# Kernel optimization log

Measured on AMD Instinct MI355X. Metric: run time of the kernel, lower is better.

## Reference

```python
import jax, jax.numpy as jnp
import numpy as np

N = 50000      # nodes
E = 800000     # edges (avg degree 16)
DIN = 256      # input_dim
DH = 128       # hidden_dim
ALPHA_LOGIT = 0.6190392084062235  # logit(0.65)


def setup_inputs() -> dict:
    key = jax.random.key(0)
    ks = jax.random.split(key, 12)
    f = lambda k, s: jax.random.normal(k, s, dtype=jnp.float32)
    return {
        "x": f(ks[0], (N, DIN)),
        "edge_index": jax.random.randint(ks[1], (2, E), 0, N, dtype=jnp.int32),
        "reranker_scores": f(ks[2], (N,)),
        # input_proj
        "Wp": f(ks[3], (DIN, DH)) * 0.02, "bp": jnp.zeros((DH,), jnp.float32),
        # SAGEConv 0: lin_l (aggregated neighbors, with bias), lin_r (root, no bias)
        "Wl0": f(ks[4], (DIN, DH)) * 0.02, "bl0": jnp.zeros((DH,), jnp.float32),
        "Wr0": f(ks[5], (DIN, DH)) * 0.02,
        # SAGEConv 1
        "Wl1": f(ks[6], (DH, DH)) * 0.02, "bl1": jnp.zeros((DH,), jnp.float32),
        "Wr1": f(ks[7], (DH, DH)) * 0.02,
        # score head MLP
        "W1": f(ks[8], (DH, DH // 2)) * 0.02, "b1": jnp.zeros((DH // 2,), jnp.float32),
        "W2": f(ks[9], (DH // 2, 1)) * 0.02, "b2": jnp.zeros((1,), jnp.float32),
        "alpha_logit": jnp.float32(ALPHA_LOGIT),
    }


def _sage_conv(h, src, dst, Wl, bl, Wr):
    # PyG SAGEConv (aggr='mean', root_weight=True):
    # out = lin_l(mean_{j in N(i)} h_j) + lin_r(h_i)
    msg = h[src]                                             # [E, d] gather
    agg = jax.ops.segment_sum(msg, dst, num_segments=N)      # [N, d]
    cnt = jax.ops.segment_sum(jnp.ones((src.shape[0],), h.dtype), dst, num_segments=N)
    agg = agg / jnp.maximum(cnt, 1.0)[:, None]               # mean; isolated nodes -> 0
    return agg @ Wl + bl + h @ Wr


def reference(x, edge_index, reranker_scores, Wp, bp, Wl0, bl0, Wr0,
              Wl1, bl1, Wr1, W1, b1, W2, b2, alpha_logit):
    src, dst = edge_index[0], edge_index[1]
    # norm_type='none' -> no input normalization; eval mode -> dropout is identity
    residual = x @ Wp + bp                                   # [N, DH]
    h = jax.nn.relu(_sage_conv(x, src, dst, Wl0, bl0, Wr0)) + residual
    h = jax.nn.relu(_sage_conv(h, src, dst, Wl1, bl1, Wr1)) + h
    gnn_scores = (jax.nn.relu(h @ W1 + b1) @ W2 + b2)[:, 0]  # [N]
    alpha = jax.nn.sigmoid(alpha_logit)
    return alpha * reranker_scores + (1.0 - alpha) * gnn_scores
```

## Files before the change

kernel.cpp:

```cpp
#include <hip/hip_runtime.h>
#include <hip/hip_bf16.h>


#define DIN 256
#define DH 128
#define NPB 256
#define LOG_NPB 8
#define NBMAX 256
#define EPB 2048
#define JL (EPB/256)
#define SLOTS 8192

typedef __attribute__((ext_vector_type(8))) short short8;
typedef __attribute__((ext_vector_type(4))) float float4v;
typedef __attribute__((ext_vector_type(2))) float float2v;

__device__ inline ushort f2b(float f){
  unsigned u = __float_as_uint(f);
  u = (u + 0x7fffu + ((u >> 16) & 1u)) >> 16;
  return (ushort)u;
}
__device__ inline float blo(unsigned v){ return __uint_as_float(v << 16); }
__device__ inline float bhi(unsigned v){ return __uint_as_float(v & 0xffff0000u); }
__device__ inline short8 pack8(float4 f0, float4 f1){
  short8 v;
  v[0]=(short)f2b(f0.x); v[1]=(short)f2b(f0.y); v[2]=(short)f2b(f0.z); v[3]=(short)f2b(f0.w);
  v[4]=(short)f2b(f1.x); v[5]=(short)f2b(f1.y); v[6]=(short)f2b(f1.z); v[7]=(short)f2b(f1.w);
  return v;
}
__device__ inline void glds16(const ushort* g, ushort* l){
  __builtin_amdgcn_global_load_lds((const __attribute__((address_space(1))) void*)g,
                                   (__attribute__((address_space(3))) void*)l, 16, 0, 0);
}
__device__ inline unsigned char enc8(float v){
  return (unsigned char)(__builtin_amdgcn_cvt_pk_fp8_f32(v, v, 0, false) & 0xFF);
}
__device__ inline float2v dec8(unsigned u){
  return __builtin_amdgcn_cvt_pk_f32_fp8((int)u, false);
}

__device__ inline void gather16x2(const ushort* __restrict__ a8,
    const int* __restrict__ adj, int pA, int eA, int pB, int eB, int lane,
    float2v& aA, float2v& aB)
{
  while (pA < eA || pB < eB){
    ushort uA[16], uB[16];
    bool dA = pA < eA, dB = pB < eB;
    if (dA){
      #pragma unroll
      for (int j=0;j<16;j++){
        int ix = __builtin_amdgcn_readfirstlane(adj[pA+j]);
        uA[j] = a8[(size_t)ix*64 + lane];
      }
    }
    if (dB){
      #pragma unroll
      for (int j=0;j<16;j++){
        int ix = __builtin_amdgcn_readfirstlane(adj[pB+j]);
        uB[j] = a8[(size_t)ix*64 + lane];
      }
    }
    if (dA){
      #pragma unroll
      for (int j=0;j<16;j++) aA += dec8(uA[j]);
      pA += 16;
    }
    if (dB){
      #pragma unroll
      for (int j=0;j<16;j++) aB += dec8(uB[j]);
      pB += 16;
    }
  }
}

__global__ __launch_bounds__(256) void fused_front(
    const float* __restrict__ x, int N, ushort* __restrict__ xb, int nstripe,
    const float* __restrict__ Wp, const float* __restrict__ Wl0, const float* __restrict__ Wr0,
    const float* __restrict__ Wl1, const float* __restrict__ Wr1, const float* __restrict__ W1,
    ushort* __restrict__ Wpf, ushort* __restrict__ Wl0f, ushort* __restrict__ Wr0f,
    ushort* __restrict__ Wl1f, ushort* __restrict__ Wr1f, ushort* __restrict__ W1f,
    const int* __restrict__ src, const int* __restrict__ dst, int E, int NB,
    int* __restrict__ bucketCnt, int* __restrict__ pairS, int* __restrict__ pairD,
    int nPart, int nConv)
{
  __shared__ int hist[NBMAX], lbase[NBMAX], gbase[NBMAX], lcur[NBMAX], sc[NBMAX];
  __shared__ int ls[EPB], ld[EPB];
  int bid = blockIdx.x;
  int t = threadIdx.x;

  if (bid < nPart){
    int base = bid * EPB;
    int cntE = E - base; if (cntE > EPB) cntE = EPB;
    for (int i=t;i<NB;i+=256) hist[i]=0;
    __syncthreads();
    int myS[JL], myD[JL];
    #pragma unroll
    for (int j=0;j<JL;j++){
      int e = base + j*256 + t;
      if (e < E){ myS[j]=src[e]; myD[j]=dst[e]; atomicAdd(&hist[myD[j]>>LOG_NPB],1); }
      else myD[j] = -1;
    }
    __syncthreads();
    if (t < NBMAX) sc[t] = (t < NB)? hist[t] : 0;
    __syncthreads();
    for (int st=1; st<NBMAX; st<<=1){
      int v = 0;
      if (t < NBMAX && t >= st) v = sc[t-st];
      __syncthreads();
      if (t < NBMAX) sc[t] += v;
      __syncthreads();
    }
    if (t < NB){
      int excl = (t>0)? sc[t-1] : 0;
      lbase[t] = excl; lcur[t] = excl;
      gbase[t] = atomicAdd(&bucketCnt[t], hist[t]);
    }
    __syncthreads();
    #pragma unroll
    for (int j=0;j<JL;j++){
      if (myD[j] >= 0){
        int b = myD[j] >> LOG_NPB;
        int p = atomicAdd(&lcur[b], 1);
        ls[p] = myS[j]; ld[p] = myD[j];
      }
    }
    __syncthreads();
    for (int i=t;i<cntE;i+=256){
      int d = ld[i];
      int b = d >> LOG_NPB;
      int p = gbase[b] + (i - lbase[b]);
      if (p < SLOTS){
        pairS[(size_t)b*SLOTS + p] = ls[i];
        pairD[(size_t)b*SLOTS + p] = d;
      }
    }
  } else if (bid < nPart + nConv){
    int gi = (bid - nPart)*256 + t;
    if (gi < nstripe*512){
      int L = gi & 63, ks = (gi>>6)&7, s = gi>>9;
      int row = s*16 + (L&15);
      int k = ks*32 + (L>>4)*8;
      short8 v;
      if (row < N){
        const float* p = x + (size_t)row*DIN + k;
        v = pack8(*(const float4*)p, *(const float4*)(p+4));
      } else {
        #pragma unroll
        for (int j=0;j<8;j++) v[j]=0;
      }
      *(short8*)(xb + (size_t)gi*8) = v;
    }
  } else {
    int gi = (bid - nPart - nConv)*256 + t;
    if (gi < 17408){
      const float* sw; ushort* dw; int cols, b0;
      if      (gi <  4096){ sw=Wp;  dw=Wpf;  cols=128; b0=0; }
      else if (gi <  8192){ sw=Wl0; dw=Wl0f; cols=128; b0=4096; }
      else if (gi < 12288){ sw=Wr0; dw=Wr0f; cols=128; b0=8192; }
      else if (gi < 14336){ sw=Wl1; dw=Wl1f; cols=128; b0=12288; }
      else if (gi < 16384){ sw=Wr1; dw=Wr1f; cols=128; b0=14336; }
      else                { sw=W1;  dw=W1f;  cols=64;  b0=16384; }
      int i = gi - b0;
      int ln = i & 63, g = i >> 6;
      int ntq = cols >> 4;
      int nt = g % ntq, ks = g / ntq;
      int col = nt*16 + (ln & 15);
      int k0 = ks*32 + (ln >> 4)*8;
      short8 v;
      #pragma unroll
      for (int j=0;j<8;j++) v[j] = (short)f2b(sw[(size_t)(k0+j)*cols + col]);
      *(short8*)(dw + (size_t)i*8) = v;
    }
  }
}

__global__ __launch_bounds__(256) void gemm0_csr(
    const ushort* __restrict__ xb, int N, int nstripe, int ngemm, int nbuck,
    const ushort* __restrict__ Wpf, const ushort* __restrict__ Wl0f, const ushort* __restrict__ Wr0f,
    const float* __restrict__ bp,
    ushort* __restrict__ xp, unsigned char* __restrict__ q8, ushort* __restrict__ xr0,
    const int* __restrict__ bucketCnt, const int* __restrict__ pairS, const int* __restrict__ pairD,
    int* __restrict__ off, int* __restrict__ deg, int* __restrict__ adj)
{
  __shared__ __align__(16) ushort smem[32768];
  int bid = blockIdx.x, t = threadIdx.x;

  if (bid >= nbuck){
    int g = bid - nbuck;
    int xcd = g & 7, jj = g >> 3;
    int mat = jj % 3;
    int b = xcd + 8*(jj/3);
    int nblk = ngemm / 3;
    const ushort* Wf = (mat==0)? Wpf : (mat==1)? Wl0f : Wr0f;
    int w = t>>6, lane = t&63, lq = lane&15, quad = lane>>4;
    #pragma unroll
    for (int j=0;j<16;j++){
      int gg = w + j*4;
      glds16(Wf + (size_t)gg*512 + lane*8, smem + gg*512);
    }
    __syncthreads();
    float bias[8];
    #pragma unroll
    for (int nt=0;nt<8;nt++) bias[nt] = (mat==0)? bp[nt*16 + lq] : 0.f;
    int nchunk = (nstripe + 3) >> 2;

#define LOADAV(AV, cc) do { \
    int stripe_ = (cc)*4 + w; \
    if (stripe_ < nstripe){ \
      _Pragma("unroll") \
      for (int ks=0;ks<8;ks++) \
        AV[ks] = *(const short8*)(xb + ((size_t)stripe_*8 + ks)*512 + lane*8); \
    } \
  } while(0)

#define COMPSTORE(AV, cc) do { \
    int stripe_ = (cc)*4 + w; \
    if (stripe_ < nstripe){ \
      int row0_ = stripe_*16; \
      float4v acc_[8]; \
      _Pragma("unroll") for (int nt=0;nt<8;nt++){ \
        _Pragma("unroll") for (int r=0;r<4;r++) acc_[nt][r]=0.f; } \
      _Pragma("unroll") for (int ks=0;ks<8;ks++){ \
        _Pragma("unroll") for (int nt=0;nt<8;nt++){ \
          short8 bf_ = *(const short8*)(smem + (size_t)((ks*8+nt)*64 + lane)*8); \
          acc_[nt] = __builtin_amdgcn_mfma_f32_16x16x32_bf16(AV[ks], bf_, acc_[nt], 0,0,0); \
        } \
      } \
      if (mat == 1){ \
        _Pragma("unroll") for (int nt=0;nt<8;nt++) \
        _Pragma("unroll") for (int r=0;r<4;r++){ \
          int row_ = row0_ + quad*4 + r; \
          if (row_ < N) q8[(size_t)row_*128 + nt*16 + lq] = enc8(acc_[nt][r]); \
        } \
      } else { \
        ushort* Y_ = (mat==0)? xp : xr0; \
        _Pragma("unroll") for (int nt=0;nt<8;nt++) \
        _Pragma("unroll") for (int r=0;r<4;r++){ \
          int row_ = row0_ + quad*4 + r; \
          if (row_ < N) Y_[(size_t)row_*128 + nt*16 + lq] = f2b(acc_[nt][r] + bias[nt]); \
        } \
      } \
    } \
  } while(0)

    short8 avA[8], avB[8];
    int c = b;
    if (c < nchunk){
      LOADAV(avA, c);
      while (true){
        int cn = c + nblk;
        if (cn < nchunk) LOADAV(avB, cn);
        COMPSTORE(avA, c);
        c = cn;
        if (c >= nchunk) break;
        cn = c + nblk;
        if (cn < nchunk) LOADAV(avA, cn);
        COMPSTORE(avB, c);
        c = cn;
        if (c >= nchunk) break;
      }
    }
#undef LOADAV
#undef COMPSTORE
  } else {
    int b = bid;
    int* cnt  = (int*)smem;
    int* offl = cnt + 256;
    int* s1   = offl + 257;
    int* win  = s1 + 256;
    int node0 = b * NPB;
    int base  = b * SLOTS;
    int ce = bucketCnt[b]; if (ce > SLOTS) ce = SLOTS;
    int ce4 = ce & ~3;
    cnt[t] = 0;
    __syncthreads();
    for (int i = t*4; i < ce4; i += 1024){
      int4 dd = *(const int4*)(pairD + base + i);
      atomicAdd(&cnt[dd.x - node0], 1);
      atomicAdd(&cnt[dd.y - node0], 1);
      atomicAdd(&cnt[dd.z - node0], 1);
      atomicAdd(&cnt[dd.w - node0], 1);
    }
    for (int i = ce4 + t; i < ce; i += 256)
      atomicAdd(&cnt[pairD[(size_t)base+i] - node0], 1);
    __syncthreads();
    int a = cnt[t];
    int pa = (a + 15) & ~15;
    s1[t] = pa;
    __syncthreads();
    for (int st=1; st<256; st<<=1){
      int v = (t>=st)? s1[t-st] : 0;
      __syncthreads();
      s1[t] += v;
      __syncthreads();
    }
    int excl = (t>0)? s1[t-1] : 0;
    offl[t] = excl;
    int ptotal = s1[255]; if (ptotal > SLOTS) ptotal = SLOTS;
    int node = node0 + t;
    if (node < N){ off[node] = base + excl; deg[node] = a; }
    __syncthreads();
    for (int i=t;i<ptotal;i+=256) win[i] = N;
    __syncthreads();
    for (int i = t*4; i < ce4; i += 1024){
      int4 dd = *(const int4*)(pairD + base + i);
      int4 ss = *(const int4*)(pairS + base + i);
      int p0 = atomicAdd(&offl[dd.x - node0], 1); if (p0 < SLOTS) win[p0] = ss.x;
      int p1 = atomicAdd(&offl[dd.y - node0], 1); if (p1 < SLOTS) win[p1] = ss.y;
      int p2 = atomicAdd(&offl[dd.z - node0], 1); if (p2 < SLOTS) win[p2] = ss.z;
      int p3 = atomicAdd(&offl[dd.w - node0], 1); if (p3 < SLOTS) win[p3] = ss.w;
    }
    for (int i = ce4 + t; i < ce; i += 256){
      int dd = pairD[(size_t)base+i];
      int p = atomicAdd(&offl[dd - node0], 1);
      if (p < SLOTS) win[p] = pairS[(size_t)base+i];
    }
    __syncthreads();
    for (int i=t;i<ptotal;i+=256) adj[(size_t)base+i] = win[i];
  }
}

__global__ __launch_bounds__(256) void combine0_f8(
    const unsigned char* __restrict__ agg8, const ushort* __restrict__ rootsrc,
    const ushort* __restrict__ ressrc, const float* __restrict__ bias,
    const int* __restrict__ off, const int* __restrict__ deg,
    const int* __restrict__ adj, ushort* __restrict__ out, int n)
{
  int t = threadIdx.x;
  int d = t & 63, w = t >> 6;
  int nA = blockIdx.x*8 + w*2, nB = nA + 1;
  if (nA >= n) return;
  const ushort* a8 = (const ushort*)agg8;
  bool vB = nB < n;
  unsigned rtA = ((const unsigned*)rootsrc)[(size_t)nA*64 + d];
  unsigned rsA = ((const unsigned*)ressrc)[(size_t)nA*64 + d];
  unsigned rtB = 0, rsB = 0;
  int pA = off[nA], cA = deg[nA], eA = pA + ((cA + 15) & ~15);
  int pB = 0, cB = 0, eB = 0;
  if (vB){
    rtB = ((const unsigned*)rootsrc)[(size_t)nB*64 + d];
    rsB = ((const unsigned*)ressrc)[(size_t)nB*64 + d];
    pB = off[nB]; cB = deg[nB]; eB = pB + ((cB + 15) & ~15);
  }
  float2v aA = {0.f, 0.f}, aB = {0.f, 0.f};
  gather16x2(a8, adj, pA, eA, pB, eB, d, aA, aB);
  float b0 = bias[2*d], b1v = bias[2*d+1];
  float invA = 1.f / (float)((cA > 1)? cA : 1);
  float o0 = fmaxf(aA[0]*invA + b0  + blo(rtA), 0.f) + blo(rsA);
  float o1 = fmaxf(aA[1]*invA + b1v + bhi(rtA), 0.f) + bhi(rsA);
  ((unsigned*)out)[(size_t)nA*64 + d] = (unsigned)f2b(o0) | ((unsigned)f2b(o1) << 16);
  if (vB){
    float invB = 1.f / (float)((cB > 1)? cB : 1);
    float q0 = fmaxf(aB[0]*invB + b0  + blo(rtB), 0.f) + blo(rsB);
    float q1 = fmaxf(aB[1]*invB + b1v + bhi(rtB), 0.f) + bhi(rsB);
    ((unsigned*)out)[(size_t)nB*64 + d] = (unsigned)f2b(q0) | ((unsigned)f2b(q1) << 16);
  }
}

__global__ __launch_bounds__(256) void gemm1_wres(
    const ushort* __restrict__ h, int N,
    const ushort* __restrict__ Wl1f, const ushort* __restrict__ Wr1f,
    unsigned char* __restrict__ q8, ushort* __restrict__ hr1)
{
  __shared__ __align__(16) ushort Bs[32768];
  int t = threadIdx.x, w = t>>6, lane = t&63, lq = lane&15, quad = lane>>4;
  int tile = blockIdx.x;
  #pragma unroll
  for (int j=0;j<16;j++){
    int r = w + j*4;
    int m = r>>5, g = r&31;
    const ushort* Wm = m ? Wr1f : Wl1f;
    glds16(Wm + (size_t)g*512 + lane*8, Bs + r*512);
  }
  short8 av[2][4];
  int row0 = tile*128 + w*32;
  #pragma unroll
  for (int mt=0;mt<2;mt++){
    int row = row0 + mt*16 + lq; if (row >= N) row = N-1;
    #pragma unroll
    for (int ks=0;ks<4;ks++)
      av[mt][ks] = *(const short8*)(h + (size_t)row*128 + ks*32 + quad*8);
  }
  __syncthreads();
  #pragma unroll
  for (int m=0;m<2;m++){
    float4v acc[2][8];
    #pragma unroll
    for (int i=0;i<2;i++)
      #pragma unroll
      for (int j=0;j<8;j++)
        #pragma unroll
        for (int r=0;r<4;r++) acc[i][j][r] = 0.f;
    #pragma unroll
    for (int ks=0;ks<4;ks++){
      #pragma unroll
      for (int nt=0;nt<8;nt++){
        short8 bf = *(const short8*)(Bs + ((m*32 + ks*8 + nt)*64 + lane)*8);
        acc[0][nt] = __builtin_amdgcn_mfma_f32_16x16x32_bf16(av[0][ks], bf, acc[0][nt], 0,0,0);
        acc[1][nt] = __builtin_amdgcn_mfma_f32_16x16x32_bf16(av[1][ks], bf, acc[1][nt], 0,0,0);
      }
    }
    #pragma unroll
    for (int mt=0;mt<2;mt++){
      #pragma unroll
      for (int r=0;r<4;r++){
        int row = row0 + mt*16 + quad*4 + r;
        if (row < N){
          if (m == 0){
            #pragma unroll
            for (int nt=0;nt<8;nt++)
              q8[(size_t)row*128 + nt*16 + lq] = enc8(acc[mt][nt][r]);
          } else {
            #pragma unroll
            for (int nt=0;nt<8;nt++)
              hr1[(size_t)row*128 + nt*16 + lq] = f2b(acc[mt][nt][r]);
          }
        }
      }
    }
  }
}

__global__ __launch_bounds__(256) void combine1_head(
    const unsigned char* __restrict__ agg8, const ushort* __restrict__ hr1,
    const ushort* __restrict__ h, const float* __restrict__ bl1,
    const int* __restrict__ off, const int* __restrict__ deg, const int* __restrict__ adj,
    const ushort* __restrict__ W1f, const float* __restrict__ b1,
    const float* __restrict__ W2, const float* __restrict__ b2,
    const float* __restrict__ alogit, const float* __restrict__ rer,
    float* __restrict__ out, int n)
{
  __shared__ __align__(16) ushort W1s[8192];
  __shared__ __align__(16) ushort h2s[16*136];
  int t = threadIdx.x, w = t>>6, lane = t&63, lq = lane&15, quad = lane>>4;
  #pragma unroll
  for (int j=0;j<4;j++){
    int g = w + j*4;
    glds16(W1f + (size_t)g*512 + lane*8, W1s + g*512);
  }
  int node0 = blockIdx.x*16;
  unsigned* h2u = (unsigned*)h2s;
  const ushort* a8 = (const ushort*)agg8;
  float bb0 = bl1[2*lane], bb1 = bl1[2*lane+1];
  #pragma unroll
  for (int jp=0;jp<2;jp++){
    int nA = node0 + w*4 + jp*2, nB = nA + 1;
    bool vA = nA < n, vB = nB < n;
    unsigned rtA=0, rsA=0, rtB=0, rsB=0;
    int pA=0, eA=0, cA=0, pB=0, eB=0, cB=0;
    if (vA){
      rtA = ((const unsigned*)hr1)[(size_t)nA*64 + lane];
      rsA = ((const unsigned*)h  )[(size_t)nA*64 + lane];
      pA = off[nA]; cA = deg[nA]; eA = pA + ((cA + 15) & ~15);
    }
    if (vB){
      rtB = ((const unsigned*)hr1)[(size_t)nB*64 + lane];
      rsB = ((const unsigned*)h  )[(size_t)nB*64 + lane];
      pB = off[nB]; cB = deg[nB]; eB = pB + ((cB + 15) & ~15);
    }
    float2v aA = {0.f, 0.f}, aB = {0.f, 0.f};
    gather16x2(a8, adj, pA, eA, pB, eB, lane, aA, aB);
    float o0A=0.f, o1A=0.f, o0B=0.f, o1B=0.f;
    if (vA){
      float inv = 1.f / (float)((cA > 1)? cA : 1);
      o0A = fmaxf(aA[0]*inv + bb0 + blo(rtA), 0.f) + blo(rsA);
      o1A = fmaxf(aA[1]*inv + bb1 + bhi(rtA), 0.f) + bhi(rsA);
    }
    if (vB){
      float inv = 1.f / (float)((cB > 1)? cB : 1);
      o0B = fmaxf(aB[0]*inv + bb0 + blo(rtB), 0.f) + blo(rsB);
      o1B = fmaxf(aB[1]*inv + bb1 + bhi(rtB), 0.f) + bhi(rsB);
    }
    h2u[(w*4 + jp*2    )*68 + lane] = (unsigned)f2b(o0A) | ((unsigned)f2b(o1A) << 16);
    h2u[(w*4 + jp*2 + 1)*68 + lane] = (unsigned)f2b(o0B) | ((unsigned)f2b(o1B) << 16);
  }
  __syncthreads();

  short8 av[4];
  #pragma unroll
  for (int ks=0;ks<4;ks++)
    av[ks] = *(const short8*)(h2s + lq*136 + ks*32 + quad*8);
  float4v acc[4];
  #pragma unroll
  for (int nt=0;nt<4;nt++)
    #pragma unroll
    for (int r=0;r<4;r++) acc[nt][r] = 0.f;
  #pragma unroll
  for (int ks=0;ks<4;ks++){
    #pragma unroll
    for (int nt=0;nt<4;nt++){
      short8 bf = *(const short8*)(W1s + ((ks*4 + nt)*64 + lane)*8);
      acc[nt] = __builtin_amdgcn_mfma_f32_16x16x32_bf16(av[ks], bf, acc[nt], 0,0,0);
    }
  }
  float al = alogit[0];
  float a  = 1.f / (1.f + __expf(-al));
  float pw[4] = {0.f,0.f,0.f,0.f};
  #pragma unroll
  for (int nt=0; nt<4; nt++){
    int c = nt*16 + lq;
    float w2 = W2[c];
    float bb = b1[c];
    #pragma unroll
    for (int r=0; r<4; r++)
      pw[r] += fmaxf(acc[nt][r] + bb, 0.f) * w2;
  }
  #pragma unroll
  for (int mask=1; mask<16; mask<<=1){
    #pragma unroll
    for (int r=0; r<4; r++)
      pw[r] += __shfl_xor(pw[r], mask);
  }
  if (lq == 0){
    #pragma unroll
    for (int r=0; r<4; r++){
      int rl = quad*4 + r;
      if ((rl >> 2) == w){
        int node = node0 + rl;
        if (node < n)
          out[node] = a * rer[node] + (1.f - a) * (pw[r] + b2[0]);
      }
    }
  }
}

extern "C" void kernel_launch(void* const* d_in, const int* in_sizes, int n_in,
                              void* d_out, int out_size, void* d_ws, size_t ws_size,
                              hipStream_t stream)
{
  (void)n_in; (void)out_size; (void)ws_size;
  const float* x    = (const float*)d_in[0];
  const int*   ei   = (const int*)d_in[1];
  const float* rer  = (const float*)d_in[2];
  const float* Wp   = (const float*)d_in[3];
  const float* bp   = (const float*)d_in[4];
  const float* Wl0  = (const float*)d_in[5];
  const float* bl0  = (const float*)d_in[6];
  const float* Wr0  = (const float*)d_in[7];
  const float* Wl1  = (const float*)d_in[8];
  const float* bl1  = (const float*)d_in[9];
  const float* Wr1  = (const float*)d_in[10];
  const float* W1   = (const float*)d_in[11];
  const float* b1   = (const float*)d_in[12];
  const float* W2   = (const float*)d_in[13];
  const float* b2   = (const float*)d_in[14];
  const float* alogit = (const float*)d_in[15];

  const int N = in_sizes[2];
  const int E = in_sizes[1] / 2;
  const int* src = ei;
  const int* dst = ei + E;
  const int NB = (N + NPB - 1) / NPB;
  const int nstripe = (N + 15) / 16;
  const int ntile = (N + 127) / 128;
  const int nPart = (E + EPB - 1) / EPB;
  const int nConv = (nstripe*512 + 255)/256;

  ushort* U = (ushort*)d_ws;
  ushort* xb  = U;
  ushort* xp  = xb + (size_t)nstripe*512*8;
  ushort* xr0 = xp  + (size_t)N*DH;
  ushort* h   = xr0 + (size_t)N*DH;
  unsigned char* q8 = (unsigned char*)(h + (size_t)N*DH);
  ushort* Wpf  = (ushort*)(q8 + (size_t)(N+1)*DH);
  ushort* Wl0f = Wpf  + (size_t)4096*8;
  ushort* Wr0f = Wl0f + (size_t)4096*8;
  ushort* Wl1f = Wr0f + (size_t)4096*8;
  ushort* Wr1f = Wl1f + (size_t)2048*8;
  ushort* W1f  = Wr1f + (size_t)2048*8;
  int* I = (int*)(W1f + (size_t)1024*8);
  int* bucketCnt = I;
  int* off   = bucketCnt + NBMAX;
  int* deg   = off + N;
  int* pairS = deg + N;
  int* pairD = pairS + (size_t)NB*SLOTS;
  int* adj   = pairD + (size_t)NB*SLOTS;

  hipMemsetAsync(bucketCnt, 0, NBMAX*sizeof(int), stream);
  hipMemsetAsync(q8 + (size_t)N*DH, 0, DH, stream);

  fused_front<<<nPart + nConv + 68, 256, 0, stream>>>(
      x, N, xb, nstripe, Wp, Wl0, Wr0, Wl1, Wr1, W1,
      Wpf, Wl0f, Wr0f, Wl1f, Wr1f, W1f,
      src, dst, E, NB, bucketCnt, pairS, pairD, nPart, nConv);

  gemm0_csr<<<NB + 768, 256, 0, stream>>>(
      xb, N, nstripe, 768, NB, Wpf, Wl0f, Wr0f, bp, xp, q8, xr0,
      bucketCnt, pairS, pairD, off, deg, adj);

  combine0_f8<<<(N+7)/8, 256, 0, stream>>>(q8, xr0, xp, bl0, off, deg, adj, h, N);

  gemm1_wres<<<ntile, 256, 0, stream>>>(h, N, Wl1f, Wr1f, q8, xr0);

  combine1_head<<<(N+15)/16, 256, 0, stream>>>(
      q8, xr0, h, bl1, off, deg, adj, W1f, b1, W2, b2, alogit, rer, (float*)d_out, N);
}
```

Baseline: 227.4 us.

## Store CSR adjacency as 16-bit indices and split combine1 into combine plus head MLP

Result: faster. 218.3 us (median of 3 runs) (-4.0%).

```diff
diff --git a/kernel.cpp b/kernel.cpp
--- a/kernel.cpp
+++ b/kernel.cpp
@@ -40,7 +40,7 @@
 }
 
 __device__ inline void gather16x2(const ushort* __restrict__ a8,
-    const int* __restrict__ adj, int pA, int eA, int pB, int eB, int lane,
+    const ushort* __restrict__ adj, int pA, int eA, int pB, int eB, int lane,
     float2v& aA, float2v& aB)
 {
   while (pA < eA || pB < eB){
@@ -49,14 +49,14 @@
     if (dA){
       #pragma unroll
       for (int j=0;j<16;j++){
-        int ix = __builtin_amdgcn_readfirstlane(adj[pA+j]);
+        int ix = __builtin_amdgcn_readfirstlane((int)adj[pA+j]);
         uA[j] = a8[(size_t)ix*64 + lane];
       }
     }
     if (dB){
       #pragma unroll
       for (int j=0;j<16;j++){
-        int ix = __builtin_amdgcn_readfirstlane(adj[pB+j]);
+        int ix = __builtin_amdgcn_readfirstlane((int)adj[pB+j]);
         uB[j] = a8[(size_t)ix*64 + lane];
       }
     }
@@ -180,7 +180,7 @@
     const float* __restrict__ bp,
     ushort* __restrict__ xp, unsigned char* __restrict__ q8, ushort* __restrict__ xr0,
     const int* __restrict__ bucketCnt, const int* __restrict__ pairS, const int* __restrict__ pairD,
-    int* __restrict__ off, int* __restrict__ deg, int* __restrict__ adj)
+    int* __restrict__ off, int* __restrict__ deg, ushort* __restrict__ adj)
 {
   __shared__ __align__(16) ushort smem[32768];
   int bid = blockIdx.x, t = threadIdx.x;
@@ -267,7 +267,7 @@
     int* cnt  = (int*)smem;
     int* offl = cnt + 256;
     int* s1   = offl + 257;
-    int* win  = s1 + 256;
+    ushort* win = (ushort*)(s1 + 256);
     int node0 = b * NPB;
     int base  = b * SLOTS;
     int ce = bucketCnt[b]; if (ce > SLOTS) ce = SLOTS;
@@ -300,20 +300,20 @@
     int node = node0 + t;
     if (node < N){ off[node] = base + excl; deg[node] = a; }
     __syncthreads();
-    for (int i=t;i<ptotal;i+=256) win[i] = N;
+    for (int i=t;i<ptotal;i+=256) win[i] = (ushort)N;
     __syncthreads();
     for (int i = t*4; i < ce4; i += 1024){
       int4 dd = *(const int4*)(pairD + base + i);
       int4 ss = *(const int4*)(pairS + base + i);
-      int p0 = atomicAdd(&offl[dd.x - node0], 1); if (p0 < SLOTS) win[p0] = ss.x;
-      int p1 = atomicAdd(&offl[dd.y - node0], 1); if (p1 < SLOTS) win[p1] = ss.y;
-      int p2 = atomicAdd(&offl[dd.z - node0], 1); if (p2 < SLOTS) win[p2] = ss.z;
-      int p3 = atomicAdd(&offl[dd.w - node0], 1); if (p3 < SLOTS) win[p3] = ss.w;
+      int p0 = atomicAdd(&offl[dd.x - node0], 1); if (p0 < SLOTS) win[p0] = (ushort)ss.x;
+      int p1 = atomicAdd(&offl[dd.y - node0], 1); if (p1 < SLOTS) win[p1] = (ushort)ss.y;
+      int p2 = atomicAdd(&offl[dd.z - node0], 1); if (p2 < SLOTS) win[p2] = (ushort)ss.z;
+      int p3 = atomicAdd(&offl[dd.w - node0], 1); if (p3 < SLOTS) win[p3] = (ushort)ss.w;
     }
     for (int i = ce4 + t; i < ce; i += 256){
       int dd = pairD[(size_t)base+i];
       int p = atomicAdd(&offl[dd - node0], 1);
-      if (p < SLOTS) win[p] = pairS[(size_t)base+i];
+      if (p < SLOTS) win[p] = (ushort)pairS[(size_t)base+i];
     }
     __syncthreads();
     for (int i=t;i<ptotal;i+=256) adj[(size_t)base+i] = win[i];
@@ -324,7 +324,7 @@
     const unsigned char* __restrict__ agg8, const ushort* __restrict__ rootsrc,
     const ushort* __restrict__ ressrc, const float* __restrict__ bias,
     const int* __restrict__ off, const int* __restrict__ deg,
-    const int* __restrict__ adj, ushort* __restrict__ out, int n)
+    const ushort* __restrict__ adj, ushort* __restrict__ out, int n)
 {
   int t = threadIdx.x;
   int d = t & 63, w = t >> 6;
@@ -421,104 +421,72 @@
   }
 }
 
-__global__ __launch_bounds__(256) void combine1_head(
-    const unsigned char* __restrict__ agg8, const ushort* __restrict__ hr1,
-    const ushort* __restrict__ h, const float* __restrict__ bl1,
-    const int* __restrict__ off, const int* __restrict__ deg, const int* __restrict__ adj,
+__global__ __launch_bounds__(256) void head_mlp(
+    const ushort* __restrict__ h2, int n,
     const ushort* __restrict__ W1f, const float* __restrict__ b1,
     const float* __restrict__ W2, const float* __restrict__ b2,
     const float* __restrict__ alogit, const float* __restrict__ rer,
-    float* __restrict__ out, int n)
+    float* __restrict__ out)
 {
   __shared__ __align__(16) ushort W1s[8192];
-  __shared__ __align__(16) ushort h2s[16*136];
   int t = threadIdx.x, w = t>>6, lane = t&63, lq = lane&15, quad = lane>>4;
   #pragma unroll
   for (int j=0;j<4;j++){
     int g = w + j*4;
     glds16(W1f + (size_t)g*512 + lane*8, W1s + g*512);
   }
-  int node0 = blockIdx.x*16;
-  unsigned* h2u = (unsigned*)h2s;
-  const ushort* a8 = (const ushort*)agg8;
-  float bb0 = bl1[2*lane], bb1 = bl1[2*lane+1];
-  #pragma unroll
-  for (int jp=0;jp<2;jp++){
-    int nA = node0 + w*4 + jp*2, nB = nA + 1;
-    bool vA = nA < n, vB = nB < n;
-    unsigned rtA=0, rsA=0, rtB=0, rsB=0;
-    int pA=0, eA=0, cA=0, pB=0, eB=0, cB=0;
-    if (vA){
-      rtA = ((const unsigned*)hr1)[(size_t)nA*64 + lane];
-      rsA = ((const unsigned*)h  )[(size_t)nA*64 + lane];
-      pA = off[nA]; cA = deg[nA]; eA = pA + ((cA + 15) & ~15);
-    }
-    if (vB){
-      rtB = ((const unsigned*)hr1)[(size_t)nB*64 + lane];
-      rsB = ((const unsigned*)h  )[(size_t)nB*64 + lane];
-      pB = off[nB]; cB = deg[nB]; eB = pB + ((cB + 15) & ~15);
-    }
-    float2v aA = {0.f, 0.f}, aB = {0.f, 0.f};
-    gather16x2(a8, adj, pA, eA, pB, eB, lane, aA, aB);
-    float o0A=0.f, o1A=0.f, o0B=0.f, o1B=0.f;
-    if (vA){
-      float inv = 1.f / (float)((cA > 1)? cA : 1);
-      o0A = fmaxf(aA[0]*inv + bb0 + blo(rtA), 0.f) + blo(rsA);
-      o1A = fmaxf(aA[1]*inv + bb1 + bhi(rtA), 0.f) + bhi(rsA);
-    }
-    if (vB){
-      float inv = 1.f / (float)((cB > 1)? cB : 1);
-      o0B = fmaxf(aB[0]*inv + bb0 + blo(rtB), 0.f) + blo(rsB);
-      o1B = fmaxf(aB[1]*inv + bb1 + bhi(rtB), 0.f) + bhi(rsB);
-    }
-    h2u[(w*4 + jp*2    )*68 + lane] = (unsigned)f2b(o0A) | ((unsigned)f2b(o1A) << 16);
-    h2u[(w*4 + jp*2 + 1)*68 + lane] = (unsigned)f2b(o0B) | ((unsigned)f2b(o1B) << 16);
+  int row0 = blockIdx.x*128 + w*32;
+  short8 av[2][4];
+  #pragma unroll
+  for (int mt=0;mt<2;mt++){
+    int row = row0 + mt*16 + lq; if (row >= n) row = n-1;
+    #pragma unroll
+    for (int ks=0;ks<4;ks++)
+      av[mt][ks] = *(const short8*)(h2 + (size_t)row*128 + ks*32 + quad*8);
   }
   __syncthreads();
-
-  short8 av[4];
-  #pragma unroll
-  for (int ks=0;ks<4;ks++)
-    av[ks] = *(const short8*)(h2s + lq*136 + ks*32 + quad*8);
-  float4v acc[4];
-  #pragma unroll
-  for (int nt=0;nt<4;nt++)
-    #pragma unroll
-    for (int r=0;r<4;r++) acc[nt][r] = 0.f;
+  float4v acc[2][4];
+  #pragma unroll
+  for (int mt=0;mt<2;mt++)
+    #pragma unroll
+    for (int nt=0;nt<4;nt++)
+      #pragma unroll
+      for (int r=0;r<4;r++) acc[mt][nt][r] = 0.f;
   #pragma unroll
   for (int ks=0;ks<4;ks++){
     #pragma unroll
     for (int nt=0;nt<4;nt++){
       short8 bf = *(const short8*)(W1s + ((ks*4 + nt)*64 + lane)*8);
-      acc[nt] = __builtin_amdgcn_mfma_f32_16x16x32_bf16(av[ks], bf, acc[nt], 0,0,0);
+      acc[0][nt] = __builtin_amdgcn_mfma_f32_16x16x32_bf16(av[0][ks], bf, acc[0][nt], 0,0,0);
+      acc[1][nt] = __builtin_amdgcn_mfma_f32_16x16x32_bf16(av[1][ks], bf, acc[1][nt], 0,0,0);
     }
   }
   float al = alogit[0];
   float a  = 1.f / (1.f + __expf(-al));
-  float pw[4] = {0.f,0.f,0.f,0.f};
-  #pragma unroll
-  for (int nt=0; nt<4; nt++){
-    int c = nt*16 + lq;
-    float w2 = W2[c];
-    float bb = b1[c];
-    #pragma unroll
-    for (int r=0; r<4; r++)
-      pw[r] += fmaxf(acc[nt][r] + bb, 0.f) * w2;
-  }
-  #pragma unroll
-  for (int mask=1; mask<16; mask<<=1){
-    #pragma unroll
-    for (int r=0; r<4; r++)
-      pw[r] += __shfl_xor(pw[r], mask);
-  }
-  if (lq == 0){
-    #pragma unroll
-    for (int r=0; r<4; r++){
-      int rl = quad*4 + r;
-      if ((rl >> 2) == w){
-        int node = node0 + rl;
-        if (node < n)
-          out[node] = a * rer[node] + (1.f - a) * (pw[r] + b2[0]);
+  #pragma unroll
+  for (int mt=0;mt<2;mt++){
+    float pw[4] = {0.f,0.f,0.f,0.f};
+    #pragma unroll
+    for (int nt=0; nt<4; nt++){
+      int c = nt*16 + lq;
+      float w2 = W2[c];
+      float bb = b1[c];
+      #pragma unroll
+      for (int r=0; r<4; r++)
+        pw[r] += fmaxf(acc[mt][nt][r] + bb, 0.f) * w2;
+    }
+    #pragma unroll
+    for (int mask=1; mask<16; mask<<=1){
+      #pragma unroll
+      for (int r=0; r<4; r++)
+        pw[r] += __shfl_xor(pw[r], mask);
+    }
+    if (lq == 0){
+      #pragma unroll
+      for (int r=0; r<4; r++){
+        int row = row0 + mt*16 + quad*4 + r;
+        if (row < n)
+          out[row] = a * rer[row] + (1.f - a) * (pw[r] + b2[0]);
       }
     }
   }
@@ -574,7 +542,8 @@
   int* deg   = off + N;
   int* pairS = deg + N;
   int* pairD = pairS + (size_t)NB*SLOTS;
-  int* adj   = pairD + (size_t)NB*SLOTS;
+  ushort* adj = (ushort*)(pairD + (size_t)NB*SLOTS);
+  ushort* h2  = xb;
 
   hipMemsetAsync(bucketCnt, 0, NBMAX*sizeof(int), stream);
   hipMemsetAsync(q8 + (size_t)N*DH, 0, DH, stream);
@@ -592,6 +561,7 @@
 
   gemm1_wres<<<ntile, 256, 0, stream>>>(h, N, Wl1f, Wr1f, q8, xr0);
 
-  combine1_head<<<(N+15)/16, 256, 0, stream>>>(
-      q8, xr0, h, bl1, off, deg, adj, W1f, b1, W2, b2, alogit, rer, (float*)d_out, N);
-}
+  combine0_f8<<<(N+7)/8, 256, 0, stream>>>(q8, xr0, h, bl1, off, deg, adj, h2, N);
+
+  head_mlp<<<ntile, 256, 0, stream>>>(h2, N, W1f, b1, W2, b2, alogit, rer, (float*)d_out);
+}
```
